# Kernel tuning notes

Measured on AMD Instinct MI355X. Metric: run time of the kernel, lower is better.

The kernel has to match this reference:

```python
import jax, jax.numpy as jnp
import numpy as np

N = 8192
IN_F = 512
OUT_F = 128
NUM_CLASSES = 10
ALPHA = 0.2  # LeakyReLU negative slope
NEG_INF = -9e15


def setup_inputs() -> dict:
    key = jax.random.key(0)
    k_h, k_d, k_W, k_a, k_cw, k_cb = jax.random.split(key, 6)
    h = jax.random.normal(k_h, (N, IN_F), dtype=jnp.float32)
    dist = jax.random.randint(k_d, (N, N), 0, 2, dtype=jnp.int32)
    # xavier_uniform with gain=1.414
    gain = 1.414
    lim_W = gain * np.sqrt(6.0 / (IN_F + OUT_F))
    W = jax.random.uniform(k_W, (IN_F, OUT_F), minval=-lim_W, maxval=lim_W, dtype=jnp.float32)
    lim_a = gain * np.sqrt(6.0 / (2 * OUT_F + 1))
    a = jax.random.uniform(k_a, (2 * OUT_F, 1), minval=-lim_a, maxval=lim_a, dtype=jnp.float32)
    # nn.Linear(out_features, num_classes): weight [C, out], bias [C]
    lim_c = np.sqrt(1.0 / OUT_F)
    Wc = jax.random.uniform(k_cw, (NUM_CLASSES, OUT_F), minval=-lim_c, maxval=lim_c, dtype=jnp.float32)
    bc = jax.random.uniform(k_cb, (NUM_CLASSES,), minval=-lim_c, maxval=lim_c, dtype=jnp.float32)
    return {"h": h, "dist": dist, "W": W, "a": a, "Wc": Wc, "bc": bc}


def reference(h, dist, W, a, Wc, bc):
    Wh = h @ W                              # [N, out]
    Wh1 = Wh @ a[:OUT_F]                    # [N, 1]
    Wh2 = Wh @ a[OUT_F:]                    # [N, 1]
    e = jax.nn.leaky_relu(Wh1 + Wh2.T, negative_slope=ALPHA)  # [N, N]
    att = jnp.where(dist > 0, e, NEG_INF)
    att = jax.nn.softmax(att, axis=1)       # [N, N]
    h_update = jax.nn.elu(att @ Wh)         # [N, out] (dropout inactive at inference)
    y_pred = h_update @ Wc.T + bc           # [N, num_classes]
    return y_pred
```

## Files before the change

kernel.cpp:

```cpp
#include <hip/hip_runtime.h>
#include <stdint.h>

#define N 8192
#define IN_F 512
#define OUT_F 128
#define NCLS 10
#define ALPHA 0.2f

typedef float f32x4 __attribute__((ext_vector_type(4)));
typedef int   i32x4 __attribute__((ext_vector_type(4)));
typedef short s16x4 __attribute__((ext_vector_type(4)));
typedef short s16x8 __attribute__((ext_vector_type(8)));

__device__ __forceinline__ short f2bf(float x) {
    unsigned u = __builtin_bit_cast(unsigned, x);
    u = (u + 0x7FFFu + ((u >> 16) & 1u)) >> 16;
    return (short)u;
}
__device__ __forceinline__ float bf2f(short s) {
    unsigned u = ((unsigned)(unsigned short)s) << 16;
    return __builtin_bit_cast(float, u);
}

__global__ void split_w_kernel(const float* __restrict__ W,
                               short* __restrict__ WThi, short* __restrict__ WTlo) {
    int idx = blockIdx.x * 256 + threadIdx.x;
    int k = idx >> 7, col = idx & 127;
    float x = W[idx];
    short hi = f2bf(x);
    short lo = f2bf(x - bf2f(hi));
    size_t a = (size_t)(k >> 5) * (128 * 32) + (size_t)col * 32 + (k & 31);
    WThi[a] = hi;
    WTlo[a] = lo;
}

#define WH_ROWS 16
#define WH_STR 520

__global__ __launch_bounds__(256, 2)
void wh_kernel(const float* __restrict__ h, const short* __restrict__ WThi,
               const short* __restrict__ WTlo, const float* __restrict__ a,
               short* __restrict__ WhT, float* __restrict__ Wh1,
               float* __restrict__ Wh2) {
    __shared__ __align__(16) short Ahi[WH_ROWS][WH_STR];
    __shared__ __align__(16) short Alo[WH_ROWS][WH_STR];
    __shared__ __align__(16) float whs[WH_ROWS][OUT_F + 4];

    const int t = threadIdx.x;
    const int r0 = blockIdx.x * WH_ROWS;

    {
        int row = t >> 4, c4 = t & 15;
        const float* hrow = h + (size_t)(r0 + row) * IN_F;
        #pragma unroll
        for (int jj = 0; jj < 4; ++jj) {
            int k0 = c4 * 8 + jj * 128;
            f32x4 x0 = *(const f32x4*)(hrow + k0);
            f32x4 x1 = *(const f32x4*)(hrow + k0 + 4);
            s16x8 hi, lo;
            #pragma unroll
            for (int e = 0; e < 4; ++e) {
                short h0 = f2bf(x0[e]); hi[e] = h0; lo[e] = f2bf(x0[e] - bf2f(h0));
                short h1 = f2bf(x1[e]); hi[4 + e] = h1; lo[4 + e] = f2bf(x1[e] - bf2f(h1));
            }
            *(s16x8*)&Ahi[row][k0] = hi;
            *(s16x8*)&Alo[row][k0] = lo;
        }
    }
    __syncthreads();

    const int lane = t & 63, w = t >> 6;
    const int q = lane >> 4, ln16 = lane & 15;
    f32x4 acc[2] = {};
    #pragma unroll
    for (int kc = 0; kc < IN_F / 32; ++kc) {
        s16x8 ahi = *(const s16x8*)&Ahi[ln16][kc * 32 + q * 8];
        s16x8 alo = *(const s16x8*)&Alo[ln16][kc * 32 + q * 8];
        #pragma unroll
        for (int nt = 0; nt < 2; ++nt) {
            int col = w * 32 + nt * 16 + ln16;
            size_t boff = (size_t)kc * 4096 + (size_t)col * 32 + q * 8;
            s16x8 bhi = *(const s16x8*)(WThi + boff);
            s16x8 blo = *(const s16x8*)(WTlo + boff);
            acc[nt] = __builtin_amdgcn_mfma_f32_16x16x32_bf16(ahi, bhi, acc[nt], 0, 0, 0);
            acc[nt] = __builtin_amdgcn_mfma_f32_16x16x32_bf16(ahi, blo, acc[nt], 0, 0, 0);
            acc[nt] = __builtin_amdgcn_mfma_f32_16x16x32_bf16(alo, bhi, acc[nt], 0, 0, 0);
        }
    }
    #pragma unroll
    for (int nt = 0; nt < 2; ++nt)
        #pragma unroll
        for (int reg = 0; reg < 4; ++reg)
            whs[q * 4 + reg][w * 32 + nt * 16 + ln16] = acc[nt][reg];
    __syncthreads();

    if (t < 128) {
        int r = t >> 3, s = t & 7;
        float s1 = 0.f, s2 = 0.f;
        #pragma unroll
        for (int cc = 0; cc < 16; ++cc) {
            int c = s * 16 + cc;
            float v = whs[r][c];
            s1 = fmaf(v, a[c], s1);
            s2 = fmaf(v, a[OUT_F + c], s2);
        }
        s1 += __shfl_xor(s1, 1); s1 += __shfl_xor(s1, 2); s1 += __shfl_xor(s1, 4);
        s2 += __shfl_xor(s2, 1); s2 += __shfl_xor(s2, 2); s2 += __shfl_xor(s2, 4);
        if (s == 0) { Wh1[r0 + r] = s1; Wh2[r0 + r] = s2; }
    }

    {
        int c = t >> 1, h8 = t & 1;
        s16x8 pack;
        #pragma unroll
        for (int rr = 0; rr < 8; ++rr) pack[rr] = f2bf(whs[h8 * 8 + rr][c]);
        size_t addr = (size_t)(r0 >> 5) * 4096 + (size_t)c * 32 + (r0 & 16) + h8 * 8;
        *(s16x8*)(WhT + addr) = pack;
    }
}

#define BM 32
#define BK 256
#define ASTR (BK + 8)

__global__ __launch_bounds__(256, 4)
void attn_kernel(const int* __restrict__ dist, const short* __restrict__ WhT,
                 const float* __restrict__ Wh1v, const float* __restrict__ Wh2v,
                 float* __restrict__ acc_part, float* __restrict__ l_part,
                 int nit) {
    __shared__ __align__(16) short As[2][BM][ASTR];

    const int t = threadIdx.x;
    const int it = blockIdx.x & 255;
    const int sp = blockIdx.x >> 8;
    const int i0 = it * BM;
    const int r = t >> 3, s = t & 7;
    const int lane = t & 63, w = t >> 6;
    const int q = lane >> 4, ln16 = lane & 15;
    const int j0 = sp * nit * BK;

    const int* __restrict__ drow = dist + (size_t)(i0 + r) * N + j0;
    const float* __restrict__ wh2p = Wh2v + j0;
    const float wh1 = Wh1v[i0 + r];
    float l_acc = 0.f;
    f32x4 acc[2][2] = {};

    i32x4 d[8];
    #pragma unroll
    for (int u = 0; u < 8; ++u) d[u] = *(const i32x4*)(drow + u * 32 + s * 4);

    for (int kt = 0; kt < nit; ++kt) {
        const int jb = kt * BK;
        const bool more = (kt + 1) < nit;
        i32x4 dn[8];
        if (more) {
            #pragma unroll
            for (int u = 0; u < 8; ++u)
                dn[u] = *(const i32x4*)(drow + jb + BK + u * 32 + s * 4);
        }
        short* arow = &As[kt & 1][r][0];
        #pragma unroll
        for (int u = 0; u < 8; ++u) {
            f32x4 w2 = *(const f32x4*)(wh2p + jb + u * 32 + s * 4);
            s16x4 pk;
            #pragma unroll
            for (int e = 0; e < 4; ++e) {
                float sv = wh1 + w2[e];
                float lr = fmaxf(sv, ALPHA * sv);
                float pv = (d[u][e] > 0) ? __expf(lr) : 0.f;
                l_acc += pv;
                pk[e] = f2bf(pv);
            }
            *(s16x4*)(arow + u * 32 + s * 4) = pk;
        }
        __syncthreads();
        const short* ab = &As[kt & 1][0][0];
        const short* bbase = WhT + (size_t)(j0 + jb) * 128;
        #pragma unroll
        for (int kc = 0; kc < BK / 32; ++kc) {
            s16x8 a0 = *(const s16x8*)(ab + ln16 * ASTR + kc * 32 + q * 8);
            s16x8 a1 = *(const s16x8*)(ab + (16 + ln16) * ASTR + kc * 32 + q * 8);
            #pragma unroll
            for (int nt = 0; nt < 2; ++nt) {
                int col = w * 32 + nt * 16 + ln16;
                s16x8 b = *(const s16x8*)(bbase + (size_t)kc * 4096 + col * 32 + q * 8);
                acc[0][nt] = __builtin_amdgcn_mfma_f32_16x16x32_bf16(a0, b, acc[0][nt], 0, 0, 0);
                acc[1][nt] = __builtin_amdgcn_mfma_f32_16x16x32_bf16(a1, b, acc[1][nt], 0, 0, 0);
            }
        }
        if (more) {
            #pragma unroll
            for (int u = 0; u < 8; ++u) d[u] = dn[u];
        }
    }

    l_acc += __shfl_xor(l_acc, 1);
    l_acc += __shfl_xor(l_acc, 2);
    l_acc += __shfl_xor(l_acc, 4);
    if (s == 0) l_part[(size_t)sp * N + i0 + r] = l_acc;

    float* ap = acc_part + (size_t)sp * N * OUT_F + (size_t)i0 * OUT_F;
    #pragma unroll
    for (int mt = 0; mt < 2; ++mt)
        #pragma unroll
        for (int reg = 0; reg < 4; ++reg) {
            int row = mt * 16 + q * 4 + reg;
            #pragma unroll
            for (int nt = 0; nt < 2; ++nt)
                ap[(size_t)row * OUT_F + w * 32 + nt * 16 + ln16] = acc[mt][nt][reg];
        }
}

__global__ __launch_bounds__(256, 4)
void reduce_kernel(const float* __restrict__ acc_part, const float* __restrict__ l_part,
                   const float* __restrict__ Wc, const float* __restrict__ bcv,
                   float* __restrict__ out, int split) {
    __shared__ __align__(16) float hu[16][OUT_F + 4];
    const int t = threadIdx.x;
    const int i0 = blockIdx.x * 16;
    const int row = t >> 4, cg = t & 15;

    f32x4 v0 = {0.f, 0.f, 0.f, 0.f}, v1 = {0.f, 0.f, 0.f, 0.f};
    float l = 0.f;
    for (int s = 0; s < split; ++s) {
        const float* ap = acc_part + (size_t)s * N * OUT_F + (size_t)(i0 + row) * OUT_F + cg * 8;
        v0 += *(const f32x4*)ap;
        v1 += *(const f32x4*)(ap + 4);
        l += l_part[(size_t)s * N + i0 + row];
    }
    float inv = 1.f / l;
    #pragma unroll
    for (int e = 0; e < 4; ++e) {
        float x0 = v0[e] * inv; x0 = x0 > 0.f ? x0 : (__expf(x0) - 1.f);
        float x1 = v1[e] * inv; x1 = x1 > 0.f ? x1 : (__expf(x1) - 1.f);
        hu[row][cg * 8 + e] = x0;
        hu[row][cg * 8 + 4 + e] = x1;
    }
    __syncthreads();

    if (t < 16 * NCLS) {
        int rr = t / NCLS, cls = t - rr * NCLS;
        const f32x4* hurow = (const f32x4*)&hu[rr][0];
        const f32x4* wcrow = (const f32x4*)(Wc + cls * OUT_F);
        float sum = bcv[cls];
        #pragma unroll 8
        for (int c4 = 0; c4 < OUT_F / 4; ++c4) {
            f32x4 hv = hurow[c4];
            f32x4 wv = wcrow[c4];
            sum += hv[0] * wv[0] + hv[1] * wv[1] + hv[2] * wv[2] + hv[3] * wv[3];
        }
        out[(size_t)(i0 + rr) * NCLS + cls] = sum;
    }
}

extern "C" void kernel_launch(void* const* d_in, const int* in_sizes, int n_in,
                              void* d_out, int out_size, void* d_ws, size_t ws_size,
                              hipStream_t stream) {
    const float* h    = (const float*)d_in[0];
    const int*   dist = (const int*)d_in[1];
    const float* W    = (const float*)d_in[2];
    const float* a    = (const float*)d_in[3];
    const float* Wc   = (const float*)d_in[4];
    const float* bc   = (const float*)d_in[5];
    float* out = (float*)d_out;

    char* ws = (char*)d_ws;
    size_t off = 0;
    short* WhT  = (short*)(ws + off); off += (size_t)OUT_F * N * 2;
    short* WThi = (short*)(ws + off); off += (size_t)IN_F * OUT_F * 2;
    short* WTlo = (short*)(ws + off); off += (size_t)IN_F * OUT_F * 2;
    float* Wh1  = (float*)(ws + off); off += (size_t)N * 4;
    float* Wh2  = (float*)(ws + off); off += (size_t)N * 4;

    size_t per_split = (size_t)N * OUT_F * 4 + (size_t)N * 4;
    int split = 4;
    if (off + 4 * per_split > ws_size) split = 2;
    if (off + 2 * per_split > ws_size) split = 1;
    float* acc_part = (float*)(ws + off); off += (size_t)split * N * OUT_F * 4;
    float* l_part   = (float*)(ws + off);

    hipLaunchKernelGGL(split_w_kernel, dim3(256), dim3(256), 0, stream, W, WThi, WTlo);
    hipLaunchKernelGGL(wh_kernel, dim3(N / WH_ROWS), dim3(256), 0, stream,
                       h, WThi, WTlo, a, WhT, Wh1, Wh2);
    int nit = N / (BK * split);
    hipLaunchKernelGGL(attn_kernel, dim3(256 * split), dim3(256), 0, stream,
                       dist, WhT, Wh1, Wh2, acc_part, l_part, nit);
    hipLaunchKernelGGL(reduce_kernel, dim3(N / 16), dim3(256), 0, stream,
                       acc_part, l_part, Wc, bc, out, split);
}
```

Baseline: 445.6 us.

## Fuse all four GAT stages into one cooperative kernel with grid syncs

Replaces the four separate launches (weight split, Wh projection, attention, reduce) with a single cooperative kernel of 1024 blocks that runs each stage in turn, separated by grid.sync(). The aim is to remove kernel launch gaps and tail idle time between stages. The shared memory buffer is reused across stages, and the multi-launch path remains as a fallback if the cooperative launch fails. Risks are grid-barrier overhead, and the grid must be fully co-resident (1024 blocks at 4 per CU) or the launch will fail.

```diff
diff --git a/kernel.cpp b/kernel.cpp
--- a/kernel.cpp
+++ b/kernel.cpp
@@ -1,5 +1,8 @@
 #include <hip/hip_runtime.h>
+#include <hip/hip_cooperative_groups.h>
 #include <stdint.h>
+
+namespace cg = cooperative_groups;
 
 #define N 8192
 #define IN_F 512
@@ -7,6 +10,17 @@
 #define NCLS 10
 #define ALPHA 0.2f
 
+#define SPLIT 4
+#define BM 32
+#define BK 256
+#define ASTR 264
+#define NIT (N / (BK * SPLIT))
+
+#define WH_ROWS 16
+#define WH_STR 520
+
+#define GRID_BLKS 1024
+
 typedef float f32x4 __attribute__((ext_vector_type(4)));
 typedef int   i32x4 __attribute__((ext_vector_type(4)));
 typedef short s16x4 __attribute__((ext_vector_type(4)));
@@ -20,6 +34,232 @@
 __device__ __forceinline__ float bf2f(short s) {
     unsigned u = ((unsigned)(unsigned short)s) << 16;
     return __builtin_bit_cast(float, u);
+}
+
+__global__ __launch_bounds__(256, 4)
+void gat_fused(const float* __restrict__ h, const int* __restrict__ dist,
+               const float* __restrict__ W, const float* __restrict__ a,
+               const float* __restrict__ Wc, const float* __restrict__ bc,
+               float* __restrict__ out,
+               short* __restrict__ WhT, short* __restrict__ WThi,
+               short* __restrict__ WTlo, float* __restrict__ Wh1,
+               float* __restrict__ Wh2, float* __restrict__ acc_part,
+               float* __restrict__ l_part)
+{
+    cg::grid_group grid = cg::this_grid();
+    __shared__ __align__(16) char smem[2 * BM * ASTR * 2];
+    const int t = threadIdx.x;
+    const int b = blockIdx.x;
+
+    if (b < 256) {
+        int idx = b * 256 + t;
+        int k = idx >> 7, col = idx & 127;
+        float x = W[idx];
+        short hi = f2bf(x);
+        short lo = f2bf(x - bf2f(hi));
+        size_t ao = (size_t)(k >> 5) * (128 * 32) + (size_t)col * 32 + (k & 31);
+        WThi[ao] = hi;
+        WTlo[ao] = lo;
+    }
+    grid.sync();
+
+    if (b < 512) {
+        short (*Ahi)[WH_STR] = (short (*)[WH_STR])(smem);
+        short (*Alo)[WH_STR] = (short (*)[WH_STR])(smem + WH_ROWS * WH_STR * 2);
+        float (*whs)[OUT_F + 4] = (float (*)[OUT_F + 4])(smem);
+
+        const int r0 = b * WH_ROWS;
+        {
+            int row = t >> 4, c4 = t & 15;
+            const float* hrow = h + (size_t)(r0 + row) * IN_F;
+            #pragma unroll
+            for (int jj = 0; jj < 4; ++jj) {
+                int k0 = c4 * 8 + jj * 128;
+                f32x4 x0 = *(const f32x4*)(hrow + k0);
+                f32x4 x1 = *(const f32x4*)(hrow + k0 + 4);
+                s16x8 hi, lo;
+                #pragma unroll
+                for (int e = 0; e < 4; ++e) {
+                    short h0 = f2bf(x0[e]); hi[e] = h0; lo[e] = f2bf(x0[e] - bf2f(h0));
+                    short h1 = f2bf(x1[e]); hi[4 + e] = h1; lo[4 + e] = f2bf(x1[e] - bf2f(h1));
+                }
+                *(s16x8*)&Ahi[row][k0] = hi;
+                *(s16x8*)&Alo[row][k0] = lo;
+            }
+        }
+        __syncthreads();
+
+        const int lane = t & 63, w = t >> 6;
+        const int q = lane >> 4, ln16 = lane & 15;
+        f32x4 acc[2] = {};
+        #pragma unroll
+        for (int kc = 0; kc < IN_F / 32; ++kc) {
+            s16x8 ahi = *(const s16x8*)&Ahi[ln16][kc * 32 + q * 8];
+            s16x8 alo = *(const s16x8*)&Alo[ln16][kc * 32 + q * 8];
+            #pragma unroll
+            for (int nt = 0; nt < 2; ++nt) {
+                int col = w * 32 + nt * 16 + ln16;
+                size_t boff = (size_t)kc * 4096 + (size_t)col * 32 + q * 8;
+                s16x8 bhi = *(const s16x8*)(WThi + boff);
+                s16x8 blo = *(const s16x8*)(WTlo + boff);
+                acc[nt] = __builtin_amdgcn_mfma_f32_16x16x32_bf16(ahi, bhi, acc[nt], 0, 0, 0);
+                acc[nt] = __builtin_amdgcn_mfma_f32_16x16x32_bf16(ahi, blo, acc[nt], 0, 0, 0);
+                acc[nt] = __builtin_amdgcn_mfma_f32_16x16x32_bf16(alo, bhi, acc[nt], 0, 0, 0);
+            }
+        }
+        __syncthreads();
+        #pragma unroll
+        for (int nt = 0; nt < 2; ++nt)
+            #pragma unroll
+            for (int reg = 0; reg < 4; ++reg)
+                whs[q * 4 + reg][w * 32 + nt * 16 + ln16] = acc[nt][reg];
+        __syncthreads();
+
+        if (t < 128) {
+            int r = t >> 3, s = t & 7;
+            float s1 = 0.f, s2 = 0.f;
+            #pragma unroll
+            for (int cc = 0; cc < 16; ++cc) {
+                int c = s * 16 + cc;
+                float v = whs[r][c];
+                s1 = fmaf(v, a[c], s1);
+                s2 = fmaf(v, a[OUT_F + c], s2);
+            }
+            s1 += __shfl_xor(s1, 1); s1 += __shfl_xor(s1, 2); s1 += __shfl_xor(s1, 4);
+            s2 += __shfl_xor(s2, 1); s2 += __shfl_xor(s2, 2); s2 += __shfl_xor(s2, 4);
+            if (s == 0) { Wh1[r0 + r] = s1; Wh2[r0 + r] = s2; }
+        }
+        {
+            int c = t >> 1, h8 = t & 1;
+            s16x8 pack;
+            #pragma unroll
+            for (int rr = 0; rr < 8; ++rr) pack[rr] = f2bf(whs[h8 * 8 + rr][c]);
+            size_t addr = (size_t)(r0 >> 5) * 4096 + (size_t)c * 32 + (r0 & 16) + h8 * 8;
+            *(s16x8*)(WhT + addr) = pack;
+        }
+    }
+    grid.sync();
+
+    {
+        short (*As)[BM][ASTR] = (short (*)[BM][ASTR])smem;
+        const int it = b & 255;
+        const int sp = b >> 8;
+        const int i0 = it * BM;
+        const int r = t >> 3, s = t & 7;
+        const int lane = t & 63, w = t >> 6;
+        const int q = lane >> 4, ln16 = lane & 15;
+        const int j0 = sp * (NIT * BK);
+
+        const int* __restrict__ drow = dist + (size_t)(i0 + r) * N + j0;
+        const float* __restrict__ wh2p = Wh2 + j0;
+        const float wh1 = Wh1[i0 + r];
+        float l_acc = 0.f;
+        f32x4 acc[2][2] = {};
+
+        i32x4 d[8];
+        #pragma unroll
+        for (int u = 0; u < 8; ++u) d[u] = *(const i32x4*)(drow + u * 32 + s * 4);
+
+        for (int kt = 0; kt < NIT; ++kt) {
+            const int jb = kt * BK;
+            const bool more = (kt + 1) < NIT;
+            i32x4 dn[8];
+            if (more) {
+                #pragma unroll
+                for (int u = 0; u < 8; ++u)
+                    dn[u] = *(const i32x4*)(drow + jb + BK + u * 32 + s * 4);
+            }
+            short* arow = &As[kt & 1][r][0];
+            #pragma unroll
+            for (int u = 0; u < 8; ++u) {
+                f32x4 w2 = *(const f32x4*)(wh2p + jb + u * 32 + s * 4);
+                s16x4 pk;
+                #pragma unroll
+                for (int e = 0; e < 4; ++e) {
+                    float sv = wh1 + w2[e];
+                    float lr = fmaxf(sv, ALPHA * sv);
+                    float pv = (d[u][e] > 0) ? __expf(lr) : 0.f;
+                    l_acc += pv;
+                    pk[e] = f2bf(pv);
+                }
+                *(s16x4*)(arow + u * 32 + s * 4) = pk;
+            }
+            __syncthreads();
+            const short* ab = &As[kt & 1][0][0];
+            const short* bbase = WhT + (size_t)(j0 + jb) * 128;
+            #pragma unroll
+            for (int kc = 0; kc < BK / 32; ++kc) {
+                s16x8 a0 = *(const s16x8*)(ab + ln16 * ASTR + kc * 32 + q * 8);
+                s16x8 a1 = *(const s16x8*)(ab + (16 + ln16) * ASTR + kc * 32 + q * 8);
+                #pragma unroll
+                for (int nt = 0; nt < 2; ++nt) {
+                    int col = w * 32 + nt * 16 + ln16;
+                    s16x8 bb = *(const s16x8*)(bbase + (size_t)kc * 4096 + col * 32 + q * 8);
+                    acc[0][nt] = __builtin_amdgcn_mfma_f32_16x16x32_bf16(a0, bb, acc[0][nt], 0, 0, 0);
+                    acc[1][nt] = __builtin_amdgcn_mfma_f32_16x16x32_bf16(a1, bb, acc[1][nt], 0, 0, 0);
+                }
+            }
+            if (more) {
+                #pragma unroll
+                for (int u = 0; u < 8; ++u) d[u] = dn[u];
+            }
+        }
+
+        l_acc += __shfl_xor(l_acc, 1);
+        l_acc += __shfl_xor(l_acc, 2);
+        l_acc += __shfl_xor(l_acc, 4);
+        if (s == 0) l_part[(size_t)sp * N + i0 + r] = l_acc;
+
+        float* ap = acc_part + (size_t)sp * N * OUT_F + (size_t)i0 * OUT_F;
+        #pragma unroll
+        for (int mt = 0; mt < 2; ++mt)
+            #pragma unroll
+            for (int reg = 0; reg < 4; ++reg) {
+                int row = mt * 16 + q * 4 + reg;
+                #pragma unroll
+                for (int nt = 0; nt < 2; ++nt)
+                    ap[(size_t)row * OUT_F + w * 32 + nt * 16 + ln16] = acc[mt][nt][reg];
+            }
+    }
+    grid.sync();
+
+    if (b < 512) {
+        float (*hu)[OUT_F + 4] = (float (*)[OUT_F + 4])smem;
+        const int i0 = b * 16;
+        const int row = t >> 4, cg4 = t & 15;
+
+        f32x4 v0 = {0.f, 0.f, 0.f, 0.f}, v1 = {0.f, 0.f, 0.f, 0.f};
+        float l = 0.f;
+        for (int s = 0; s < SPLIT; ++s) {
+            const float* ap = acc_part + (size_t)s * N * OUT_F + (size_t)(i0 + row) * OUT_F + cg4 * 8;
+            v0 += *(const f32x4*)ap;
+            v1 += *(const f32x4*)(ap + 4);
+            l += l_part[(size_t)s * N + i0 + row];
+        }
+        float inv = 1.f / l;
+        #pragma unroll
+        for (int e = 0; e < 4; ++e) {
+            float x0 = v0[e] * inv; x0 = x0 > 0.f ? x0 : (__expf(x0) - 1.f);
+            float x1 = v1[e] * inv; x1 = x1 > 0.f ? x1 : (__expf(x1) - 1.f);
+            hu[row][cg4 * 8 + e] = x0;
+            hu[row][cg4 * 8 + 4 + e] = x1;
+        }
+        __syncthreads();
+
+        if (t < 16 * NCLS) {
+            int rr = t / NCLS, cls = t - rr * NCLS;
+            const f32x4* hurow = (const f32x4*)&hu[rr][0];
+            const f32x4* wcrow = (const f32x4*)(Wc + cls * OUT_F);
+            float sum = bc[cls];
+            #pragma unroll 8
+            for (int c4 = 0; c4 < OUT_F / 4; ++c4) {
+                f32x4 hv = hurow[c4];
+                f32x4 wv = wcrow[c4];
+                sum += hv[0] * wv[0] + hv[1] * wv[1] + hv[2] * wv[2] + hv[3] * wv[3];
+            }
+            out[(size_t)(i0 + rr) * NCLS + cls] = sum;
+        }
+    }
 }
 
 __global__ void split_w_kernel(const float* __restrict__ W,
@@ -29,13 +269,10 @@
     float x = W[idx];
     short hi = f2bf(x);
     short lo = f2bf(x - bf2f(hi));
-    size_t a = (size_t)(k >> 5) * (128 * 32) + (size_t)col * 32 + (k & 31);
-    WThi[a] = hi;
-    WTlo[a] = lo;
-}
-
-#define WH_ROWS 16
-#define WH_STR 520
+    size_t ao = (size_t)(k >> 5) * (128 * 32) + (size_t)col * 32 + (k & 31);
+    WThi[ao] = hi;
+    WTlo[ao] = lo;
+}
 
 __global__ __launch_bounds__(256, 2)
 void wh_kernel(const float* __restrict__ h, const short* __restrict__ WThi,
@@ -108,7 +345,6 @@
         s2 += __shfl_xor(s2, 1); s2 += __shfl_xor(s2, 2); s2 += __shfl_xor(s2, 4);
         if (s == 0) { Wh1[r0 + r] = s1; Wh2[r0 + r] = s2; }
     }
-
     {
         int c = t >> 1, h8 = t & 1;
         s16x8 pack;
@@ -118,10 +354,6 @@
         *(s16x8*)(WhT + addr) = pack;
     }
 }
-
-#define BM 32
-#define BK 256
-#define ASTR (BK + 8)
 
 __global__ __launch_bounds__(256, 4)
 void attn_kernel(const int* __restrict__ dist, const short* __restrict__ WhT,
@@ -183,9 +415,9 @@
             #pragma unroll
             for (int nt = 0; nt < 2; ++nt) {
                 int col = w * 32 + nt * 16 + ln16;
-                s16x8 b = *(const s16x8*)(bbase + (size_t)kc * 4096 + col * 32 + q * 8);
-                acc[0][nt] = __builtin_amdgcn_mfma_f32_16x16x32_bf16(a0, b, acc[0][nt], 0, 0, 0);
-                acc[1][nt] = __builtin_amdgcn_mfma_f32_16x16x32_bf16(a1, b, acc[1][nt], 0, 0, 0);
+                s16x8 bb = *(const s16x8*)(bbase + (size_t)kc * 4096 + col * 32 + q * 8);
+                acc[0][nt] = __builtin_amdgcn_mfma_f32_16x16x32_bf16(a0, bb, acc[0][nt], 0, 0, 0);
+                acc[1][nt] = __builtin_amdgcn_mfma_f32_16x16x32_bf16(a1, bb, acc[1][nt], 0, 0, 0);
             }
         }
         if (more) {
@@ -218,12 +450,12 @@
     __shared__ __align__(16) float hu[16][OUT_F + 4];
     const int t = threadIdx.x;
     const int i0 = blockIdx.x * 16;
-    const int row = t >> 4, cg = t & 15;
+    const int row = t >> 4, cg4 = t & 15;
 
     f32x4 v0 = {0.f, 0.f, 0.f, 0.f}, v1 = {0.f, 0.f, 0.f, 0.f};
     float l = 0.f;
     for (int s = 0; s < split; ++s) {
-        const float* ap = acc_part + (size_t)s * N * OUT_F + (size_t)(i0 + row) * OUT_F + cg * 8;
+        const float* ap = acc_part + (size_t)s * N * OUT_F + (size_t)(i0 + row) * OUT_F + cg4 * 8;
         v0 += *(const f32x4*)ap;
         v1 += *(const f32x4*)(ap + 4);
         l += l_part[(size_t)s * N + i0 + row];
@@ -233,8 +465,8 @@
     for (int e = 0; e < 4; ++e) {
         float x0 = v0[e] * inv; x0 = x0 > 0.f ? x0 : (__expf(x0) - 1.f);
         float x1 = v1[e] * inv; x1 = x1 > 0.f ? x1 : (__expf(x1) - 1.f);
-        hu[row][cg * 8 + e] = x0;
-        hu[row][cg * 8 + 4 + e] = x1;
+        hu[row][cg4 * 8 + e] = x0;
+        hu[row][cg4 * 8 + 4 + e] = x1;
     }
     __syncthreads();
 
@@ -273,18 +505,29 @@
     float* Wh2  = (float*)(ws + off); off += (size_t)N * 4;
 
     size_t per_split = (size_t)N * OUT_F * 4 + (size_t)N * 4;
-    int split = 4;
+    int split = SPLIT;
     if (off + 4 * per_split > ws_size) split = 2;
     if (off + 2 * per_split > ws_size) split = 1;
     float* acc_part = (float*)(ws + off); off += (size_t)split * N * OUT_F * 4;
     float* l_part   = (float*)(ws + off);
 
-    hipLaunchKernelGGL(split_w_kernel, dim3(256), dim3(256), 0, stream, W, WThi, WTlo);
-    hipLaunchKernelGGL(wh_kernel, dim3(N / WH_ROWS), dim3(256), 0, stream,
-                       h, WThi, WTlo, a, WhT, Wh1, Wh2);
-    int nit = N / (BK * split);
-    hipLaunchKernelGGL(attn_kernel, dim3(256 * split), dim3(256), 0, stream,
-                       dist, WhT, Wh1, Wh2, acc_part, l_part, nit);
-    hipLaunchKernelGGL(reduce_kernel, dim3(N / 16), dim3(256), 0, stream,
-                       acc_part, l_part, Wc, bc, out, split);
-}
+    hipError_t rc = hipErrorUnknown;
+    if (split == SPLIT) {
+        void* args[] = { (void*)&h, (void*)&dist, (void*)&W, (void*)&a,
+                         (void*)&Wc, (void*)&bc, (void*)&out,
+                         (void*)&WhT, (void*)&WThi, (void*)&WTlo,
+                         (void*)&Wh1, (void*)&Wh2, (void*)&acc_part, (void*)&l_part };
+        rc = hipLaunchCooperativeKernel((const void*)gat_fused, dim3(GRID_BLKS),
+                                        dim3(256), args, 0u, stream);
+    }
+    if (rc != hipSuccess) {
+        hipLaunchKernelGGL(split_w_kernel, dim3(256), dim3(256), 0, stream, W, WThi, WTlo);
+        hipLaunchKernelGGL(wh_kernel, dim3(N / WH_ROWS), dim3(256), 0, stream,
+                           h, WThi, WTlo, a, WhT, Wh1, Wh2);
+        int nit = N / (BK * split);
+        hipLaunchKernelGGL(attn_kernel, dim3(256 * split), dim3(256), 0, stream,
+                           dist, WhT, Wh1, Wh2, acc_part, l_part, nit);
+        hipLaunchKernelGGL(reduce_kernel, dim3(N / 16), dim3(256), 0, stream,
+                           acc_part, l_part, Wc, bc, out, split);
+    }
+}
```

After: 762.7 us. +71.1%, slower.

## Prepack dist adjacency into bitmask before attention kernel

Applied to the files above, without the earlier changes.

Adds a pre-pass kernel that compresses the int32 dist matrix into a 1-bit-per-entry mask. The attention kernel then reads 8 words per tile instead of 32 int32 values per thread, shrinking its load traffic and register use for prefetch. The full dist matrix is still read once, so the total bytes read stay the same, plus an extra kernel launch and the write and re-read of the mask. The intent is to decouple bandwidth from the exp/MFMA-heavy attention loop.

```diff
diff --git a/kernel.cpp b/kernel.cpp
--- a/kernel.cpp
+++ b/kernel.cpp
@@ -20,6 +20,20 @@
 __device__ __forceinline__ float bf2f(short s) {
     unsigned u = ((unsigned)(unsigned short)s) << 16;
     return __builtin_bit_cast(float, u);
+}
+
+__global__ __launch_bounds__(256, 8)
+void mask_kernel(const int* __restrict__ dist, unsigned* __restrict__ mask) {
+    size_t w = (size_t)blockIdx.x * 256 + threadIdx.x;
+    const int* p = dist + w * 32;
+    unsigned b = 0;
+    #pragma unroll
+    for (int u = 0; u < 8; ++u) {
+        i32x4 v = *(const i32x4*)(p + u * 4);
+        #pragma unroll
+        for (int e = 0; e < 4; ++e) b |= (v[e] > 0 ? 1u : 0u) << (u * 4 + e);
+    }
+    mask[w] = b;
 }
 
 __global__ void split_w_kernel(const float* __restrict__ W,
@@ -124,7 +138,7 @@
 #define ASTR (BK + 8)
 
 __global__ __launch_bounds__(256, 4)
-void attn_kernel(const int* __restrict__ dist, const short* __restrict__ WhT,
+void attn_kernel(const unsigned* __restrict__ mask, const short* __restrict__ WhT,
                  const float* __restrict__ Wh1v, const float* __restrict__ Wh2v,
                  float* __restrict__ acc_part, float* __restrict__ l_part,
                  int nit) {
@@ -138,40 +152,41 @@
     const int lane = t & 63, w = t >> 6;
     const int q = lane >> 4, ln16 = lane & 15;
     const int j0 = sp * nit * BK;
-
-    const int* __restrict__ drow = dist + (size_t)(i0 + r) * N + j0;
+    const int sh = s * 4;
+
+    const unsigned* __restrict__ mrow = mask + (size_t)(i0 + r) * (N / 32) + (j0 >> 5);
     const float* __restrict__ wh2p = Wh2v + j0;
     const float wh1 = Wh1v[i0 + r];
     float l_acc = 0.f;
     f32x4 acc[2][2] = {};
 
-    i32x4 d[8];
-    #pragma unroll
-    for (int u = 0; u < 8; ++u) d[u] = *(const i32x4*)(drow + u * 32 + s * 4);
+    i32x4 m0 = *(const i32x4*)(mrow);
+    i32x4 m1 = *(const i32x4*)(mrow + 4);
 
     for (int kt = 0; kt < nit; ++kt) {
         const int jb = kt * BK;
         const bool more = (kt + 1) < nit;
-        i32x4 dn[8];
+        i32x4 n0, n1;
         if (more) {
-            #pragma unroll
-            for (int u = 0; u < 8; ++u)
-                dn[u] = *(const i32x4*)(drow + jb + BK + u * 32 + s * 4);
+            n0 = *(const i32x4*)(mrow + (kt + 1) * 8);
+            n1 = *(const i32x4*)(mrow + (kt + 1) * 8 + 4);
         }
         short* arow = &As[kt & 1][r][0];
         #pragma unroll
         for (int u = 0; u < 8; ++u) {
-            f32x4 w2 = *(const f32x4*)(wh2p + jb + u * 32 + s * 4);
+            f32x4 w2 = *(const f32x4*)(wh2p + jb + u * 32 + sh);
+            unsigned wrd = (u < 4) ? (unsigned)m0[u] : (unsigned)m1[u - 4];
+            unsigned nib = (wrd >> sh) & 15u;
             s16x4 pk;
             #pragma unroll
             for (int e = 0; e < 4; ++e) {
                 float sv = wh1 + w2[e];
                 float lr = fmaxf(sv, ALPHA * sv);
-                float pv = (d[u][e] > 0) ? __expf(lr) : 0.f;
+                float pv = (nib & (1u << e)) ? __expf(lr) : 0.f;
                 l_acc += pv;
                 pk[e] = f2bf(pv);
             }
-            *(s16x4*)(arow + u * 32 + s * 4) = pk;
+            *(s16x4*)(arow + u * 32 + sh) = pk;
         }
         __syncthreads();
         const short* ab = &As[kt & 1][0][0];
@@ -188,10 +203,7 @@
                 acc[1][nt] = __builtin_amdgcn_mfma_f32_16x16x32_bf16(a1, b, acc[1][nt], 0, 0, 0);
             }
         }
-        if (more) {
-            #pragma unroll
-            for (int u = 0; u < 8; ++u) d[u] = dn[u];
-        }
+        if (more) { m0 = n0; m1 = n1; }
     }
 
     l_acc += __shfl_xor(l_acc, 1);
@@ -271,6 +283,7 @@
     short* WTlo = (short*)(ws + off); off += (size_t)IN_F * OUT_F * 2;
     float* Wh1  = (float*)(ws + off); off += (size_t)N * 4;
     float* Wh2  = (float*)(ws + off); off += (size_t)N * 4;
+    unsigned* mask = (unsigned*)(ws + off); off += (size_t)N * (N / 32) * 4;
 
     size_t per_split = (size_t)N * OUT_F * 4 + (size_t)N * 4;
     int split = 4;
@@ -279,12 +292,14 @@
     float* acc_part = (float*)(ws + off); off += (size_t)split * N * OUT_F * 4;
     float* l_part   = (float*)(ws + off);
 
+    hipLaunchKernelGGL(mask_kernel, dim3(N * (N / 32) / 256), dim3(256), 0, stream,
+                       dist, mask);
     hipLaunchKernelGGL(split_w_kernel, dim3(256), dim3(256), 0, stream, W, WThi, WTlo);
     hipLaunchKernelGGL(wh_kernel, dim3(N / WH_ROWS), dim3(256), 0, stream,
                        h, WThi, WTlo, a, WhT, Wh1, Wh2);
     int nit = N / (BK * split);
     hipLaunchKernelGGL(attn_kernel, dim3(256 * split), dim3(256), 0, stream,
-                       dist, WhT, Wh1, Wh2, acc_part, l_part, nit);
+                       mask, WhT, Wh1, Wh2, acc_part, l_part, nit);
     hipLaunchKernelGGL(reduce_kernel, dim3(N / 16), dim3(256), 0, stream,
                        acc_part, l_part, Wc, bc, out, split);
 }
```

Result: no change. 437.1 us (-1.9%).

## Compute attention probabilities directly in MFMA A-fragment registers, drop LDS staging

Applied to the files above, without the earlier changes.

The attention kernel now has each wave own 16 rows. Each lane computes its exp-masked attention values straight into the bf16 MFMA A operand, which removes the shared-memory tile and the __syncthreads per K-tile. Each wave covers all 128 output columns with 8 accumulators, and the block tile grows to 64 rows. The split-K factor rises to 8 when workspace allows, giving 1024 blocks. The trade-offs are less coalesced dist loads (32-byte chunks per lane across rows), more reduce traffic from the larger split, and no LDS sharing of WhT B-fragments between waves.

```diff
diff --git a/kernel.cpp b/kernel.cpp
--- a/kernel.cpp
+++ b/kernel.cpp
@@ -119,96 +119,82 @@
     }
 }
 
-#define BM 32
-#define BK 256
-#define ASTR (BK + 8)
+#define BM2 64
 
 __global__ __launch_bounds__(256, 4)
 void attn_kernel(const int* __restrict__ dist, const short* __restrict__ WhT,
                  const float* __restrict__ Wh1v, const float* __restrict__ Wh2v,
                  float* __restrict__ acc_part, float* __restrict__ l_part,
-                 int nit) {
-    __shared__ __align__(16) short As[2][BM][ASTR];
-
+                 int nkc, int jspan) {
     const int t = threadIdx.x;
-    const int it = blockIdx.x & 255;
-    const int sp = blockIdx.x >> 8;
-    const int i0 = it * BM;
-    const int r = t >> 3, s = t & 7;
-    const int lane = t & 63, w = t >> 6;
+    const int it = blockIdx.x & 127;
+    const int sp = blockIdx.x >> 7;
+    const int i0 = it * BM2;
+    const int w = t >> 6, lane = t & 63;
     const int q = lane >> 4, ln16 = lane & 15;
-    const int j0 = sp * nit * BK;
-
-    const int* __restrict__ drow = dist + (size_t)(i0 + r) * N + j0;
-    const float* __restrict__ wh2p = Wh2v + j0;
-    const float wh1 = Wh1v[i0 + r];
+    const int row = i0 + w * 16 + ln16;
+    const int j0 = sp * jspan;
+
+    const int*   __restrict__ dp = dist + (size_t)row * N + j0 + q * 8;
+    const float* __restrict__ wp = Wh2v + j0 + q * 8;
+    const float wh1 = Wh1v[row];
+    const short* __restrict__ wb0 = WhT + ((size_t)(j0 >> 5)) * 4096 + ln16 * 32 + q * 8;
+
+    f32x4 acc[8] = {};
     float l_acc = 0.f;
-    f32x4 acc[2][2] = {};
-
-    i32x4 d[8];
-    #pragma unroll
-    for (int u = 0; u < 8; ++u) d[u] = *(const i32x4*)(drow + u * 32 + s * 4);
-
-    for (int kt = 0; kt < nit; ++kt) {
-        const int jb = kt * BK;
-        const bool more = (kt + 1) < nit;
-        i32x4 dn[8];
+
+    i32x4 dA = *(const i32x4*)(dp);
+    i32x4 dB = *(const i32x4*)(dp + 4);
+    f32x4 wA = *(const f32x4*)(wp);
+    f32x4 wB = *(const f32x4*)(wp + 4);
+
+    for (int kc = 0; kc < nkc; ++kc) {
+        i32x4 dA2, dB2; f32x4 wA2, wB2;
+        const bool more = (kc + 1) < nkc;
         if (more) {
-            #pragma unroll
-            for (int u = 0; u < 8; ++u)
-                dn[u] = *(const i32x4*)(drow + jb + BK + u * 32 + s * 4);
-        }
-        short* arow = &As[kt & 1][r][0];
-        #pragma unroll
-        for (int u = 0; u < 8; ++u) {
-            f32x4 w2 = *(const f32x4*)(wh2p + jb + u * 32 + s * 4);
-            s16x4 pk;
-            #pragma unroll
-            for (int e = 0; e < 4; ++e) {
-                float sv = wh1 + w2[e];
-                float lr = fmaxf(sv, ALPHA * sv);
-                float pv = (d[u][e] > 0) ? __expf(lr) : 0.f;
-                l_acc += pv;
-                pk[e] = f2bf(pv);
-            }
-            *(s16x4*)(arow + u * 32 + s * 4) = pk;
-        }
-        __syncthreads();
-        const short* ab = &As[kt & 1][0][0];
-        const short* bbase = WhT + (size_t)(j0 + jb) * 128;
-        #pragma unroll
-        for (int kc = 0; kc < BK / 32; ++kc) {
-            s16x8 a0 = *(const s16x8*)(ab + ln16 * ASTR + kc * 32 + q * 8);
-            s16x8 a1 = *(const s16x8*)(ab + (16 + ln16) * ASTR + kc * 32 + q * 8);
-            #pragma unroll
-            for (int nt = 0; nt < 2; ++nt) {
-                int col = w * 32 + nt * 16 + ln16;
-                s16x8 b = *(const s16x8*)(bbase + (size_t)kc * 4096 + col * 32 + q * 8);
-                acc[0][nt] = __builtin_amdgcn_mfma_f32_16x16x32_bf16(a0, b, acc[0][nt], 0, 0, 0);
-                acc[1][nt] = __builtin_amdgcn_mfma_f32_16x16x32_bf16(a1, b, acc[1][nt], 0, 0, 0);
-            }
-        }
-        if (more) {
-            #pragma unroll
-            for (int u = 0; u < 8; ++u) d[u] = dn[u];
-        }
-    }
-
-    l_acc += __shfl_xor(l_acc, 1);
-    l_acc += __shfl_xor(l_acc, 2);
-    l_acc += __shfl_xor(l_acc, 4);
-    if (s == 0) l_part[(size_t)sp * N + i0 + r] = l_acc;
-
-    float* ap = acc_part + (size_t)sp * N * OUT_F + (size_t)i0 * OUT_F;
-    #pragma unroll
-    for (int mt = 0; mt < 2; ++mt)
-        #pragma unroll
-        for (int reg = 0; reg < 4; ++reg) {
-            int row = mt * 16 + q * 4 + reg;
-            #pragma unroll
-            for (int nt = 0; nt < 2; ++nt)
-                ap[(size_t)row * OUT_F + w * 32 + nt * 16 + ln16] = acc[mt][nt][reg];
-        }
+            dA2 = *(const i32x4*)(dp + (kc + 1) * 32);
+            dB2 = *(const i32x4*)(dp + (kc + 1) * 32 + 4);
+            wA2 = *(const f32x4*)(wp + (kc + 1) * 32);
+            wB2 = *(const f32x4*)(wp + (kc + 1) * 32 + 4);
+        }
+        s16x8 af;
+        #pragma unroll
+        for (int e = 0; e < 4; ++e) {
+            float sv = wh1 + wA[e];
+            float lr = fmaxf(sv, ALPHA * sv);
+            float pv = (dA[e] > 0) ? __expf(lr) : 0.f;
+            l_acc += pv;
+            af[e] = f2bf(pv);
+        }
+        #pragma unroll
+        for (int e = 0; e < 4; ++e) {
+            float sv = wh1 + wB[e];
+            float lr = fmaxf(sv, ALPHA * sv);
+            float pv = (dB[e] > 0) ? __expf(lr) : 0.f;
+            l_acc += pv;
+            af[4 + e] = f2bf(pv);
+        }
+        const short* wb = wb0 + (size_t)kc * 4096;
+        #pragma unroll
+        for (int nt = 0; nt < 8; ++nt) {
+            s16x8 b = *(const s16x8*)(wb + nt * 512);
+            acc[nt] = __builtin_amdgcn_mfma_f32_16x16x32_bf16(af, b, acc[nt], 0, 0, 0);
+        }
+        if (more) { dA = dA2; dB = dB2; wA = wA2; wB = wB2; }
+    }
+
+    l_acc += __shfl_xor(l_acc, 16);
+    l_acc += __shfl_xor(l_acc, 32);
+    if (lane < 16) l_part[(size_t)sp * N + row] = l_acc;
+
+    float* ap = acc_part + (size_t)sp * N * OUT_F + (size_t)(i0 + w * 16) * OUT_F;
+    #pragma unroll
+    for (int reg = 0; reg < 4; ++reg) {
+        int rr = q * 4 + reg;
+        #pragma unroll
+        for (int nt = 0; nt < 8; ++nt)
+            ap[(size_t)rr * OUT_F + nt * 16 + ln16] = acc[nt][reg];
+    }
 }
 
 __global__ __launch_bounds__(256, 4)
@@ -273,18 +259,17 @@
     float* Wh2  = (float*)(ws + off); off += (size_t)N * 4;
 
     size_t per_split = (size_t)N * OUT_F * 4 + (size_t)N * 4;
-    int split = 4;
-    if (off + 4 * per_split > ws_size) split = 2;
-    if (off + 2 * per_split > ws_size) split = 1;
+    int split = 8;
+    while (split > 1 && off + (size_t)split * per_split > ws_size) split >>= 1;
     float* acc_part = (float*)(ws + off); off += (size_t)split * N * OUT_F * 4;
     float* l_part   = (float*)(ws + off);
 
     hipLaunchKernelGGL(split_w_kernel, dim3(256), dim3(256), 0, stream, W, WThi, WTlo);
     hipLaunchKernelGGL(wh_kernel, dim3(N / WH_ROWS), dim3(256), 0, stream,
                        h, WThi, WTlo, a, WhT, Wh1, Wh2);
-    int nit = N / (BK * split);
-    hipLaunchKernelGGL(attn_kernel, dim3(256 * split), dim3(256), 0, stream,
-                       dist, WhT, Wh1, Wh2, acc_part, l_part, nit);
+    hipLaunchKernelGGL(attn_kernel, dim3(128 * split), dim3(256), 0, stream,
+                       dist, WhT, Wh1, Wh2, acc_part, l_part,
+                       N / (32 * split), N / split);
     hipLaunchKernelGGL(reduce_kernel, dim3(N / 16), dim3(256), 0, stream,
                        acc_part, l_part, Wc, bc, out, split);
 }
```

Measured after the change: 487.5 us. +9.4%, slower.
